# Optimization experiments

Measured on AMD Instinct MI355X. Metric: run time of the kernel, lower is better.

Reference implementation:

```python
import jax, jax.numpy as jnp
import numpy as np

B, LI, LT, DM, H = 1, 2048, 384, 2560, 20
DH = DM // H  # 128
EPS = 1e-05


def _rms(x, w):
    # torch.nn.RMSNorm over last dim (inner_dim), elementwise affine w
    return x * jax.lax.rsqrt(jnp.mean(x * x, axis=-1, keepdims=True) + EPS) * w


def _apply_rope(x, rope):
    # x: [B, L, H, D]; rope: [1, L, 1, D/2, 2, 2] (flux-style freqs_cis)
    xr = x.reshape(x.shape[0], x.shape[1], x.shape[2], -1, 1, 2)  # [B,L,H,D/2,1,2]
    out = rope[..., 0] * xr[..., 0] + rope[..., 1] * xr[..., 1]   # [B,L,H,D/2,2]
    return out.reshape(x.shape)


def _sdpa(q, k, v):
    # q,k,v: [B, L, H, D] -> out [B, L, H*D]; scale 1/sqrt(D)
    scale = 1.0 / np.sqrt(q.shape[-1]).astype(np.float32)
    scores = jnp.einsum('bqhd,bkhd->bhqk', q, k) * scale
    p = jax.nn.softmax(scores, axis=-1)
    o = jnp.einsum('bhqk,bkhd->bqhd', p, v)
    return o.reshape(o.shape[0], o.shape[1], -1)


def _lin(x, W, b):
    return x @ W.T + b


def _forward(img, txt, rope, img_masks,
             Wq, bq, Wk, bk, Wv, bv, Wo, bo, qn, kn,
             Wq_t, bq_t, Wk_t, bk_t, Wv_t, bv_t, Wo_t, bo_t, qn_t, kn_t):
    bsz = img.shape[0]
    # img stream: proj -> RMSNorm -> head split
    iq = _rms(_lin(img, Wq, bq), qn).reshape(bsz, -1, H, DH)
    ik = _rms(_lin(img, Wk, bk), kn).reshape(bsz, -1, H, DH)
    iv = _lin(img, Wv, bv).reshape(bsz, -1, H, DH)
    ik = ik * img_masks[:, :, None, None]
    # txt stream
    tq = _rms(_lin(txt, Wq_t, bq_t), qn_t).reshape(bsz, -1, H, DH)
    tk = _rms(_lin(txt, Wk_t, bk_t), kn_t).reshape(bsz, -1, H, DH)
    tv = _lin(txt, Wv_t, bv_t).reshape(bsz, -1, H, DH)
    # concat streams, apply rope, attention
    q = jnp.concatenate([iq, tq], axis=1)
    k = jnp.concatenate([ik, tk], axis=1)
    v = jnp.concatenate([iv, tv], axis=1)
    q = _apply_rope(q, rope)
    k = _apply_rope(k, rope)
    attn = _sdpa(q, k, v)  # [B, LI+LT, DM]
    img_attn, txt_attn = attn[:, :LI], attn[:, LI:]
    return _lin(img_attn, Wo, bo), _lin(txt_attn, Wo_t, bo_t)


def setup_inputs() -> dict:
    key = jax.random.key(0)
    ks = jax.random.split(key, 16)
    s = 0.02
    inp = {
        'img': jax.random.normal(ks[0], (B, LI, DM), jnp.float32),
        'txt': jax.random.normal(ks[1], (B, LT, DM), jnp.float32),
        'rope': jax.random.normal(ks[2], (1, LI + LT, 1, DH // 2, 2, 2), jnp.float32),
        'img_masks': jnp.ones((B, LI), jnp.float32),
    }
    wnames = ['Wq', 'Wk', 'Wv', 'Wo', 'Wq_t', 'Wk_t', 'Wv_t', 'Wo_t']
    for i, n in enumerate(wnames):
        inp[n] = jax.random.normal(ks[3 + i], (DM, DM), jnp.float32) * s
        inp['b' + n[1:]] = jnp.zeros((DM,), jnp.float32)
    for i, n in enumerate(['qn', 'kn', 'qn_t', 'kn_t']):
        inp[n] = jax.random.uniform(ks[11 + i], (DM,), jnp.float32, 0.5, 1.5)
    return inp


def reference(img, txt, rope, img_masks,
              Wq, bq, Wk, bk, Wv, bv, Wo, bo, qn, kn,
              Wq_t, bq_t, Wk_t, bk_t, Wv_t, bv_t, Wo_t, bo_t, qn_t, kn_t):
    return _forward(img, txt, rope, img_masks,
                    Wq, bq, Wk, bk, Wv, bv, Wo, bo, qn, kn,
                    Wq_t, bq_t, Wk_t, bk_t, Wv_t, bv_t, Wo_t, bo_t, qn_t, kn_t)
```

## Files before the change

### kernel.cpp

```cpp
#include <hip/hip_runtime.h>
#include <math.h>

#define LI 2048
#define LT 384
#define LSEQ 2432
#define DM 2560
#define NH 20
#define DH 128
#define SCALE 0.08838834764831845f
#define NKV 38

typedef __bf16 bf16x8 __attribute__((ext_vector_type(8)));
typedef __bf16 bf16x4 __attribute__((ext_vector_type(4)));
typedef __bf16 bf16x2 __attribute__((ext_vector_type(2)));
typedef float f32x4 __attribute__((ext_vector_type(4)));
typedef float f32x16 __attribute__((ext_vector_type(16)));

__device__ __forceinline__ void async_copy16(const void* gsrc, void* lds_uniform) {
    __builtin_amdgcn_global_load_lds(
        (const __attribute__((address_space(1))) unsigned int*)gsrc,
        (__attribute__((address_space(3))) unsigned int*)lds_uniform,
        16, 0, 0);
}


__global__ __launch_bounds__(256) void cvt8_kernel(
    const float* __restrict__ s0, const float* __restrict__ s1,
    const float* __restrict__ s2, const float* __restrict__ s3,
    const float* __restrict__ s4, const float* __restrict__ s5,
    const float* __restrict__ s6, const float* __restrict__ s7,
    __bf16* __restrict__ dst)
{
    const float* srcs[8] = {s0, s1, s2, s3, s4, s5, s6, s7};
    const float* s = srcs[blockIdx.y];
    __bf16* d = dst + (size_t)blockIdx.y * (size_t)DM * DM;
    int i = blockIdx.x * 256 + threadIdx.x;
    const float4* sp = (const float4*)s + (size_t)i * 2;
    float4 a = sp[0], b = sp[1];
    bf16x8 o = {(__bf16)a.x, (__bf16)a.y, (__bf16)a.z, (__bf16)a.w,
                (__bf16)b.x, (__bf16)b.y, (__bf16)b.z, (__bf16)b.w};
    *((bf16x8*)d + i) = o;
}

__global__ __launch_bounds__(256) void cvt_kernel(
    const float* __restrict__ s, __bf16* __restrict__ d, int n8)
{
    int i = blockIdx.x * 256 + threadIdx.x;
    if (i >= n8) return;
    const float4* sp = (const float4*)s + (size_t)i * 2;
    float4 a = sp[0], b = sp[1];
    bf16x8 o = {(__bf16)a.x, (__bf16)a.y, (__bf16)a.z, (__bf16)a.w,
                (__bf16)b.x, (__bf16)b.y, (__bf16)b.z, (__bf16)b.w};
    *((bf16x8*)d + i) = o;
}


__device__ __forceinline__ void gemm_core(
    const __bf16* __restrict__ Ab,
    const __bf16* __restrict__ Bb,
    const float* __restrict__ bias,
    float* __restrict__ Cb,
    __bf16* sA, __bf16* sB)
{
    const int t = threadIdx.x, wave = t >> 6, lane = t & 63;
    const int l15 = lane & 15, quad = lane >> 4;
    const int wm = wave >> 1, wn = wave & 1;

    f32x4 acc[4][4];
#pragma unroll
    for (int i = 0; i < 4; i++)
#pragma unroll
        for (int j = 0; j < 4; j++) acc[i][j] = f32x4{0.f, 0.f, 0.f, 0.f};

    size_t soff[4];
#pragma unroll
    for (int j = 0; j < 4; j++) {
        int c = j * 256 + t;
        int row = c >> 3, u = c & 7;
        soff[j] = (size_t)row * DM + ((u ^ (row & 7)) * 8);
    }

    for (int k0 = 0; k0 < DM; k0 += 64) {
        __syncthreads();
#pragma unroll
        for (int j = 0; j < 4; j++)
            async_copy16(Ab + soff[j] + k0, (char*)sA + (j * 256 + wave * 64) * 16);
#pragma unroll
        for (int j = 0; j < 4; j++)
            async_copy16(Bb + soff[j] + k0, (char*)sB + (j * 256 + wave * 64) * 16);
        __syncthreads();

#pragma unroll
        for (int ks = 0; ks < 2; ks++) {
            bf16x8 af[4], bg[4];
#pragma unroll
            for (int mt = 0; mt < 4; mt++) {
                int r = wm * 64 + mt * 16 + l15;
                af[mt] = *(const bf16x8*)(sA + r * 64 + (((quad + ks * 4) ^ (r & 7)) * 8));
            }
#pragma unroll
            for (int nt = 0; nt < 4; nt++) {
                int r = wn * 64 + nt * 16 + l15;
                bg[nt] = *(const bf16x8*)(sB + r * 64 + (((quad + ks * 4) ^ (r & 7)) * 8));
            }
#pragma unroll
            for (int mt = 0; mt < 4; mt++)
#pragma unroll
                for (int nt = 0; nt < 4; nt++)
                    acc[mt][nt] = __builtin_amdgcn_mfma_f32_16x16x32_bf16(af[mt], bg[nt], acc[mt][nt], 0, 0, 0);
        }
    }

#pragma unroll
    for (int mt = 0; mt < 4; mt++) {
        const int row = wm * 64 + mt * 16 + quad * 4;
#pragma unroll
        for (int nt = 0; nt < 4; nt++) {
            const int col = wn * 64 + nt * 16 + l15;
            const float bv = bias[col];
            float* cp = Cb + (size_t)row * DM + col;
            cp[0]        = acc[mt][nt][0] + bv;
            cp[DM]       = acc[mt][nt][1] + bv;
            cp[2 * DM]   = acc[mt][nt][2] + bv;
            cp[3 * DM]   = acc[mt][nt][3] + bv;
        }
    }
}

__device__ __forceinline__ void qkv_body(
    int nblk, int mblk,
    const __bf16* __restrict__ xbf, const __bf16* __restrict__ wbf,
    const float* __restrict__ bq, const float* __restrict__ bk, const float* __restrict__ bv,
    const float* __restrict__ bq_t, const float* __restrict__ bk_t, const float* __restrict__ bv_t,
    float* __restrict__ qraw, float* __restrict__ kraw, float* __restrict__ vraw,
    __bf16* sA, __bf16* sB)
{
    const int which = nblk / 20;
    const int nloc = (nblk % 20) * 128;
    const bool is_txt = (mblk >= 16);
    const size_t WELEM = (size_t)DM * DM;
    const int widx = which + (is_txt ? 4 : 0);
    const __bf16* W = wbf + (size_t)widx * WELEM;
    const float* bias = (which == 0) ? (is_txt ? bq_t : bq)
                      : (which == 1) ? (is_txt ? bk_t : bk)
                                     : (is_txt ? bv_t : bv);
    float* C = (which == 0) ? qraw : (which == 1) ? kraw : vraw;
    gemm_core(xbf + (size_t)mblk * 128 * DM, W + (size_t)nloc * DM, bias + nloc,
              C + (size_t)mblk * 128 * DM + nloc, sA, sB);
}

__global__ __launch_bounds__(256, 4) void gemm_qkv_a_kernel(
    const __bf16* __restrict__ xbf, const __bf16* __restrict__ wbf,
    const float* __restrict__ bq, const float* __restrict__ bk, const float* __restrict__ bv,
    const float* __restrict__ bq_t, const float* __restrict__ bk_t, const float* __restrict__ bv_t,
    float* __restrict__ qraw, float* __restrict__ kraw, float* __restrict__ vraw)
{
    __shared__ alignas(16) __bf16 sA[128 * 64];
    __shared__ alignas(16) __bf16 sB[128 * 64];
    qkv_body(blockIdx.x, blockIdx.y, xbf, wbf, bq, bk, bv, bq_t, bk_t, bv_t,
             qraw, kraw, vraw, sA, sB);
}

__global__ __launch_bounds__(256, 4) void gemm_qkv_b_kernel(
    const __bf16* __restrict__ xbf, const __bf16* __restrict__ wbf,
    const float* __restrict__ bq, const float* __restrict__ bk, const float* __restrict__ bv,
    const float* __restrict__ bq_t, const float* __restrict__ bk_t, const float* __restrict__ bv_t,
    float* __restrict__ qraw, float* __restrict__ kraw, float* __restrict__ vraw)
{
    __shared__ alignas(16) __bf16 sA[128 * 64];
    __shared__ alignas(16) __bf16 sB[128 * 64];
    qkv_body(blockIdx.x, blockIdx.y + 10, xbf, wbf, bq, bk, bv, bq_t, bk_t, bv_t,
             qraw, kraw, vraw, sA, sB);
}

__global__ __launch_bounds__(256, 4) void gemm_out_kernel(
    const __bf16* __restrict__ attnbf, const __bf16* __restrict__ wbf,
    const float* __restrict__ bo, const float* __restrict__ bo_t,
    float* __restrict__ out)
{
    __shared__ alignas(16) __bf16 sA[128 * 64];
    __shared__ alignas(16) __bf16 sB[128 * 64];
    const int nblk = blockIdx.x, mblk = blockIdx.y;
    const bool is_txt = (mblk >= 16);
    const size_t WELEM = (size_t)DM * DM;
    const __bf16* W = wbf + (size_t)(is_txt ? 7 : 3) * WELEM;
    const float* bias = (is_txt ? bo_t : bo) + nblk * 128;
    gemm_core(attnbf + (size_t)mblk * 128 * DM, W + (size_t)nblk * 128 * DM, bias,
              out + (size_t)mblk * 128 * DM + nblk * 128, sA, sB);
}


__global__ __launch_bounds__(256) void rmsrope_kernel(
    const float* __restrict__ qraw, const float* __restrict__ kraw,
    const float* __restrict__ rope, const float* __restrict__ img_masks,
    const float* __restrict__ qn, const float* __restrict__ kn,
    const float* __restrict__ qn_t, const float* __restrict__ kn_t,
    __bf16* __restrict__ qbf, __bf16* __restrict__ kbf)
{
    const int l = blockIdx.x, t = threadIdx.x;
    const int wave = t >> 6, lane = t & 63;
    const bool is_img = (l < LI);
    const float* qw = is_img ? qn : qn_t;
    const float* kw = is_img ? kn : kn_t;
    const float kmask = is_img ? img_masks[l] : 1.0f;
    const float* qr = qraw + (size_t)l * DM;
    const float* kr = kraw + (size_t)l * DM;

    float2 qv[5], kv[5];
    float sq = 0.f, sk = 0.f;
#pragma unroll
    for (int j = 0; j < 5; j++) {
        int c2 = j * 256 + t;
        qv[j] = *(const float2*)(qr + 2 * c2);
        kv[j] = *(const float2*)(kr + 2 * c2);
        sq += qv[j].x * qv[j].x + qv[j].y * qv[j].y;
        sk += kv[j].x * kv[j].x + kv[j].y * kv[j].y;
    }
#pragma unroll
    for (int m = 32; m; m >>= 1) { sq += __shfl_xor(sq, m); sk += __shfl_xor(sk, m); }
    __shared__ float redq[4], redk[4];
    if (lane == 0) { redq[wave] = sq; redk[wave] = sk; }
    __syncthreads();
    sq = redq[0] + redq[1] + redq[2] + redq[3];
    sk = redk[0] + redk[1] + redk[2] + redk[3];
    const float rq = rsqrtf(sq * (1.0f / DM) + 1e-5f);
    const float rk = rsqrtf(sk * (1.0f / DM) + 1e-5f) * kmask;

#pragma unroll
    for (int j = 0; j < 5; j++) {
        int c2 = j * 256 + t;
        int c = 2 * c2;
        float4 rp = *(const float4*)(rope + ((size_t)l * 64 + (c2 & 63)) * 4);
        float2 w2q = *(const float2*)(qw + c);
        float2 w2k = *(const float2*)(kw + c);
        float x0 = qv[j].x * rq * w2q.x, x1 = qv[j].y * rq * w2q.y;
        bf16x2 oq = {(__bf16)(rp.x * x0 + rp.y * x1), (__bf16)(rp.z * x0 + rp.w * x1)};
        *(bf16x2*)(qbf + (size_t)l * DM + c) = oq;
        float y0 = kv[j].x * rk * w2k.x, y1 = kv[j].y * rk * w2k.y;
        bf16x2 ok = {(__bf16)(rp.x * y0 + rp.y * y1), (__bf16)(rp.z * y0 + rp.w * y1)};
        *(bf16x2*)(kbf + (size_t)l * DM + c) = ok;
    }
}


__global__ __launch_bounds__(256) void transpose_cvt_kernel(
    const float* __restrict__ src, __bf16* __restrict__ dst)
{
    __shared__ float tile[32][33];
    const int c0 = blockIdx.x * 32;
    const int r0 = blockIdx.y * 32;
    const int tc = threadIdx.x & 31, tr = threadIdx.x >> 5;
#pragma unroll
    for (int j = 0; j < 4; j++)
        tile[tr + j * 8][tc] = src[(size_t)(r0 + tr + j * 8) * DM + c0 + tc];
    __syncthreads();
#pragma unroll
    for (int j = 0; j < 4; j++)
        dst[(size_t)(c0 + tr + j * 8) * LSEQ + r0 + tc] = (__bf16)tile[tc][tr + j * 8];
}


__global__ __launch_bounds__(256, 3) void flash_kernel(
    const __bf16* __restrict__ qb, const __bf16* __restrict__ kb,
    const __bf16* __restrict__ vt, __bf16* __restrict__ ob)
{
    __shared__ alignas(16) char smem[34816];
    const int head = blockIdx.x;
    const int q0 = blockIdx.y * 64;
    const int t = threadIdx.x, wave = t >> 6, lane = t & 63;
    const int s = wave >> 1, h = wave & 1;
    const int l31 = lane & 31, h5 = lane >> 5;

    bf16x8 bq8[8];
    {
        const __bf16* qp = qb + (size_t)(q0 + s * 32 + l31) * DM + head * DH;
#pragma unroll
        for (int t8 = 0; t8 < 8; t8++)
            bq8[t8] = *(const bf16x8*)(qp + t8 * 16 + h5 * 8);
    }

    int koff[4], voff[4];
#pragma unroll
    for (int j = 0; j < 4; j++) {
        int c = j * 256 + t;
        int krow = c >> 4, ku = (c & 15) ^ (krow & 7);
        koff[j] = krow * DM + head * DH + ku * 8;
        int vrow = c >> 3, vu = (c & 7) ^ (vrow & 7);
        voff[j] = (head * DH + vrow) * LSEQ + vu * 8;
    }
    const int dunit = wave * 1024;

    const __bf16* sK = (const __bf16*)smem;
    const __bf16* sV = (const __bf16*)(smem + 16384);
    const int kbase = 32 * h;

    f32x16 o[4];
#pragma unroll
    for (int dt = 0; dt < 4; dt++)
#pragma unroll
        for (int e = 0; e < 16; e++) o[dt][e] = 0.f;
    float m_i = -INFINITY, l_i = 0.f;

    for (int it = 0; it < NKV; ++it) {
        __syncthreads();
#pragma unroll
        for (int j = 0; j < 4; j++) {
            async_copy16(kb + koff[j] + (size_t)(it * 64) * DM, smem + j * 4096 + dunit);
            async_copy16(vt + voff[j] + it * 64, smem + 16384 + j * 4096 + dunit);
        }
        __syncthreads();

        f32x16 st;
#pragma unroll
        for (int e = 0; e < 16; e++) st[e] = 0.f;
        __builtin_amdgcn_s_setprio(1);
#pragma unroll
        for (int t8 = 0; t8 < 8; t8++) {
            int row = kbase + l31;
            int unit = (2 * t8 + h5) ^ (row & 7);
            bf16x8 ak = *(const bf16x8*)(sK + row * 128 + unit * 8);
            st = __builtin_amdgcn_mfma_f32_32x32x16_bf16(ak, bq8[t8], st, 0, 0, 0);
        }
        __builtin_amdgcn_s_setprio(0);

        float mx = m_i;
#pragma unroll
        for (int e = 0; e < 16; e++) { st[e] *= SCALE; mx = fmaxf(mx, st[e]); }
        mx = fmaxf(mx, __shfl_xor(mx, 32));
        const float al = __expf(m_i - mx);
        m_i = mx;
        float sum = 0.f;
#pragma unroll
        for (int e = 0; e < 16; e++) { float p = __expf(st[e] - mx); st[e] = p; sum += p; }
        sum += __shfl_xor(sum, 32);
        l_i = l_i * al + sum;
#pragma unroll
        for (int dt = 0; dt < 4; dt++)
#pragma unroll
            for (int e = 0; e < 16; e++) o[dt][e] *= al;

        bf16x8 pfrag[2];
#pragma unroll
        for (int c = 0; c < 2; c++) {
            union { bf16x2 v; unsigned u; } A, B, C, D;
            A.v = bf16x2{(__bf16)st[8 * c + 0], (__bf16)st[8 * c + 1]};
            B.v = bf16x2{(__bf16)st[8 * c + 2], (__bf16)st[8 * c + 3]};
            C.v = bf16x2{(__bf16)st[8 * c + 4], (__bf16)st[8 * c + 5]};
            D.v = bf16x2{(__bf16)st[8 * c + 6], (__bf16)st[8 * c + 7]};
            unsigned xA = __shfl_xor(A.u, 32), xB = __shfl_xor(B.u, 32);
            unsigned xC = __shfl_xor(C.u, 32), xD = __shfl_xor(D.u, 32);
            union { unsigned w[4]; bf16x8 v; } pf;
            pf.w[0] = h5 ? xC : A.u;
            pf.w[1] = h5 ? xD : B.u;
            pf.w[2] = h5 ? C.u : xA;
            pf.w[3] = h5 ? D.u : xB;
            pfrag[c] = pf.v;
        }

        __builtin_amdgcn_s_setprio(1);
#pragma unroll
        for (int dt = 0; dt < 4; dt++) {
            int row = dt * 32 + l31;
#pragma unroll
            for (int c = 0; c < 2; c++) {
                int unit = (4 * h + 2 * c + h5) ^ (row & 7);
                bf16x8 av = *(const bf16x8*)(sV + row * 64 + unit * 8);
                o[dt] = __builtin_amdgcn_mfma_f32_32x32x16_bf16(av, pfrag[c], o[dt], 0, 0, 0);
            }
        }
        __builtin_amdgcn_s_setprio(0);
    }

    __syncthreads();
    float* mlbuf = (float*)(smem + 33792);
    if (lane < 32) {
        mlbuf[((s * 2 + h) * 2 + 0) * 32 + lane] = m_i;
        mlbuf[((s * 2 + h) * 2 + 1) * 32 + lane] = l_i;
    }
    __syncthreads();
    const float pm = mlbuf[((s * 2 + (h ^ 1)) * 2 + 0) * 32 + l31];
    const float pl = mlbuf[((s * 2 + (h ^ 1)) * 2 + 1) * 32 + l31];
    const float M = fmaxf(m_i, pm);
    const float sc = __expf(m_i - M), psc = __expf(pm - M);
    const float L = l_i * sc + pl * psc;
    const float fac = sc / L;
    float* obuf = (float*)smem + s * 4224;
    if (h == 1) {
#pragma unroll
        for (int dt = 0; dt < 4; dt++)
#pragma unroll
            for (int e = 0; e < 16; e++) {
                int dout = dt * 32 + (e & 3) + 8 * (e >> 2) + 4 * h5;
                obuf[l31 * 132 + dout] = o[dt][e] * fac;
            }
    }
    __syncthreads();
    if (h == 0) {
#pragma unroll
        for (int dt = 0; dt < 4; dt++)
#pragma unroll
            for (int e = 0; e < 16; e++) {
                int dout = dt * 32 + (e & 3) + 8 * (e >> 2) + 4 * h5;
                int idx = l31 * 132 + dout;
                obuf[idx] = o[dt][e] * fac + obuf[idx];
            }
    }
    __syncthreads();
#pragma unroll
    for (int rr = 0; rr < 8; rr++) {
        int qblk = wave * 16 + h5 * 8 + rr;
        int ss = qblk >> 5, qq = qblk & 31;
        const float* src = (const float*)smem + ss * 4224 + qq * 132 + l31 * 4;
        float4 v4 = *(const float4*)src;
        bf16x4 ov = {(__bf16)v4.x, (__bf16)v4.y, (__bf16)v4.z, (__bf16)v4.w};
        *(bf16x4*)(ob + (size_t)(q0 + qblk) * DM + head * DH + l31 * 4) = ov;
    }
}


extern "C" void kernel_launch(void* const* d_in, const int* in_sizes, int n_in,
                              void* d_out, int out_size, void* d_ws, size_t ws_size,
                              hipStream_t stream) {
    const float* img       = (const float*)d_in[0];
    const float* txt       = (const float*)d_in[1];
    const float* rope      = (const float*)d_in[2];
    const float* img_masks = (const float*)d_in[3];
    const float* Wq   = (const float*)d_in[4];  const float* bq   = (const float*)d_in[5];
    const float* Wk   = (const float*)d_in[6];  const float* bk   = (const float*)d_in[7];
    const float* Wv   = (const float*)d_in[8];  const float* bv   = (const float*)d_in[9];
    const float* Wo   = (const float*)d_in[10]; const float* bo   = (const float*)d_in[11];
    const float* Wq_t = (const float*)d_in[12]; const float* bq_t = (const float*)d_in[13];
    const float* Wk_t = (const float*)d_in[14]; const float* bk_t = (const float*)d_in[15];
    const float* Wv_t = (const float*)d_in[16]; const float* bv_t = (const float*)d_in[17];
    const float* Wo_t = (const float*)d_in[18]; const float* bo_t = (const float*)d_in[19];
    const float* qn   = (const float*)d_in[20]; const float* kn   = (const float*)d_in[21];
    const float* qn_t = (const float*)d_in[22]; const float* kn_t = (const float*)d_in[23];
    float* out = (float*)d_out;

    const size_t WELEM = (size_t)DM * DM;
    const size_t XELEM = (size_t)LSEQ * DM;

    __bf16* wbf  = (__bf16*)d_ws;
    __bf16* xbf  = wbf + 8 * WELEM;
    float*  qraw = (float*)(xbf + XELEM);
    float*  kraw = qraw + XELEM;
    float*  vraw = kraw + XELEM;
    __bf16* qbf  = (__bf16*)(vraw + XELEM);
    __bf16* kbf  = qbf + XELEM;
    __bf16* vt   = kbf + XELEM;
    __bf16* attnbf = (__bf16*)qraw;

    cvt8_kernel<<<dim3((int)(WELEM / 8 / 256), 8), 256, 0, stream>>>(
        Wq, Wk, Wv, Wo, Wq_t, Wk_t, Wv_t, Wo_t, wbf);
    cvt_kernel<<<dim3((LI * DM / 8 + 255) / 256), 256, 0, stream>>>(img, xbf, LI * DM / 8);
    cvt_kernel<<<dim3((LT * DM / 8 + 255) / 256), 256, 0, stream>>>(
        txt, xbf + (size_t)LI * DM, LT * DM / 8);

    gemm_qkv_a_kernel<<<dim3(60, 10), 256, 0, stream>>>(
        xbf, wbf, bq, bk, bv, bq_t, bk_t, bv_t, qraw, kraw, vraw);
    gemm_qkv_b_kernel<<<dim3(60, 9), 256, 0, stream>>>(
        xbf, wbf, bq, bk, bv, bq_t, bk_t, bv_t, qraw, kraw, vraw);

    rmsrope_kernel<<<dim3(LSEQ), 256, 0, stream>>>(
        qraw, kraw, rope, img_masks, qn, kn, qn_t, kn_t, qbf, kbf);

    transpose_cvt_kernel<<<dim3(DM / 32, LSEQ / 32), 256, 0, stream>>>(vraw, vt);

    flash_kernel<<<dim3(NH, LSEQ / 64), 256, 0, stream>>>(qbf, kbf, vt, attnbf);

    gemm_out_kernel<<<dim3(20, 19), 256, 0, stream>>>(attnbf, wbf, bo, bo_t, out);
}
```

Baseline: 583.7 us.

## Double-buffer K tiles in flash attention, lazy rescale with exp2, merge QKV GEMM launches

```diff
diff --git a/kernel.cpp b/kernel.cpp
--- a/kernel.cpp
+++ b/kernel.cpp
@@ -8,6 +8,7 @@
 #define NH 20
 #define DH 128
 #define SCALE 0.08838834764831845f
+#define CEXP (SCALE * 1.4426950408889634f)
 #define NKV 38
 
 typedef __bf16 bf16x8 __attribute__((ext_vector_type(8)));
@@ -127,14 +128,15 @@
     }
 }
 
-__device__ __forceinline__ void qkv_body(
-    int nblk, int mblk,
+__global__ __launch_bounds__(256, 4) void gemm_qkv_kernel(
     const __bf16* __restrict__ xbf, const __bf16* __restrict__ wbf,
     const float* __restrict__ bq, const float* __restrict__ bk, const float* __restrict__ bv,
     const float* __restrict__ bq_t, const float* __restrict__ bk_t, const float* __restrict__ bv_t,
-    float* __restrict__ qraw, float* __restrict__ kraw, float* __restrict__ vraw,
-    __bf16* sA, __bf16* sB)
-{
+    float* __restrict__ qraw, float* __restrict__ kraw, float* __restrict__ vraw)
+{
+    __shared__ alignas(16) __bf16 sA[128 * 64];
+    __shared__ alignas(16) __bf16 sB[128 * 64];
+    const int nblk = blockIdx.x, mblk = blockIdx.y;
     const int which = nblk / 20;
     const int nloc = (nblk % 20) * 128;
     const bool is_txt = (mblk >= 16);
@@ -149,30 +151,6 @@
               C + (size_t)mblk * 128 * DM + nloc, sA, sB);
 }
 
-__global__ __launch_bounds__(256, 4) void gemm_qkv_a_kernel(
-    const __bf16* __restrict__ xbf, const __bf16* __restrict__ wbf,
-    const float* __restrict__ bq, const float* __restrict__ bk, const float* __restrict__ bv,
-    const float* __restrict__ bq_t, const float* __restrict__ bk_t, const float* __restrict__ bv_t,
-    float* __restrict__ qraw, float* __restrict__ kraw, float* __restrict__ vraw)
-{
-    __shared__ alignas(16) __bf16 sA[128 * 64];
-    __shared__ alignas(16) __bf16 sB[128 * 64];
-    qkv_body(blockIdx.x, blockIdx.y, xbf, wbf, bq, bk, bv, bq_t, bk_t, bv_t,
-             qraw, kraw, vraw, sA, sB);
-}
-
-__global__ __launch_bounds__(256, 4) void gemm_qkv_b_kernel(
-    const __bf16* __restrict__ xbf, const __bf16* __restrict__ wbf,
-    const float* __restrict__ bq, const float* __restrict__ bk, const float* __restrict__ bv,
-    const float* __restrict__ bq_t, const float* __restrict__ bk_t, const float* __restrict__ bv_t,
-    float* __restrict__ qraw, float* __restrict__ kraw, float* __restrict__ vraw)
-{
-    __shared__ alignas(16) __bf16 sA[128 * 64];
-    __shared__ alignas(16) __bf16 sB[128 * 64];
-    qkv_body(blockIdx.x, blockIdx.y + 10, xbf, wbf, bq, bk, bv, bq_t, bk_t, bv_t,
-             qraw, kraw, vraw, sA, sB);
-}
-
 __global__ __launch_bounds__(256, 4) void gemm_out_kernel(
     const __bf16* __restrict__ attnbf, const __bf16* __restrict__ wbf,
     const float* __restrict__ bo, const float* __restrict__ bo_t,
@@ -264,7 +242,7 @@
     const __bf16* __restrict__ qb, const __bf16* __restrict__ kb,
     const __bf16* __restrict__ vt, __bf16* __restrict__ ob)
 {
-    __shared__ alignas(16) char smem[34816];
+    __shared__ alignas(16) char smem[49152];
     const int head = blockIdx.x;
     const int q0 = blockIdx.y * 64;
     const int t = threadIdx.x, wave = t >> 6, lane = t & 63;
@@ -289,9 +267,6 @@
         voff[j] = (head * DH + vrow) * LSEQ + vu * 8;
     }
     const int dunit = wave * 1024;
-
-    const __bf16* sK = (const __bf16*)smem;
-    const __bf16* sV = (const __bf16*)(smem + 16384);
     const int kbase = 32 * h;
 
     f32x16 o[4];
@@ -299,16 +274,21 @@
     for (int dt = 0; dt < 4; dt++)
 #pragma unroll
         for (int e = 0; e < 16; e++) o[dt][e] = 0.f;
-    float m_i = -INFINITY, l_i = 0.f;
+    float m_i = -INFINITY, l_i = 0.f, mc = 0.f;
+
+#pragma unroll
+    for (int j = 0; j < 4; j++)
+        async_copy16(kb + koff[j], smem + j * 4096 + dunit);
 
     for (int it = 0; it < NKV; ++it) {
-        __syncthreads();
-#pragma unroll
-        for (int j = 0; j < 4; j++) {
-            async_copy16(kb + koff[j] + (size_t)(it * 64) * DM, smem + j * 4096 + dunit);
-            async_copy16(vt + voff[j] + it * 64, smem + 16384 + j * 4096 + dunit);
-        }
-        __syncthreads();
+        const __bf16* sK = (const __bf16*)(smem + (it & 1) * 16384);
+        const __bf16* sV = (const __bf16*)(smem + 32768);
+
+        asm volatile("s_waitcnt vmcnt(0)\n\ts_barrier" ::: "memory");
+
+#pragma unroll
+        for (int j = 0; j < 4; j++)
+            async_copy16(vt + voff[j] + it * 64, smem + 32768 + j * 4096 + dunit);
 
         f32x16 st;
 #pragma unroll
@@ -323,21 +303,37 @@
         }
         __builtin_amdgcn_s_setprio(0);
 
-        float mx = m_i;
-#pragma unroll
-        for (int e = 0; e < 16; e++) { st[e] *= SCALE; mx = fmaxf(mx, st[e]); }
-        mx = fmaxf(mx, __shfl_xor(mx, 32));
-        const float al = __expf(m_i - mx);
-        m_i = mx;
+        float pmax = st[0];
+#pragma unroll
+        for (int e = 1; e < 16; e++) pmax = fmaxf(pmax, st[e]);
+        pmax = fmaxf(pmax, __shfl_xor(pmax, 32));
+        if (!__all(pmax <= m_i + 90.0f)) {
+            const float mnew = fmaxf(m_i, pmax);
+            const float al = exp2f((m_i - mnew) * CEXP);
+            m_i = mnew; mc = mnew * CEXP;
+#pragma unroll
+            for (int dt = 0; dt < 4; dt++)
+#pragma unroll
+                for (int e = 0; e < 16; e++) o[dt][e] *= al;
+            l_i *= al;
+        }
         float sum = 0.f;
 #pragma unroll
-        for (int e = 0; e < 16; e++) { float p = __expf(st[e] - mx); st[e] = p; sum += p; }
+        for (int e = 0; e < 16; e++) {
+            float p = exp2f(st[e] * CEXP - mc);
+            st[e] = p; sum += p;
+        }
         sum += __shfl_xor(sum, 32);
-        l_i = l_i * al + sum;
-#pragma unroll
-        for (int dt = 0; dt < 4; dt++)
-#pragma unroll
-            for (int e = 0; e < 16; e++) o[dt][e] *= al;
+        l_i += sum;
+
+        asm volatile("s_waitcnt vmcnt(0)\n\ts_barrier" ::: "memory");
+
+        if (it + 1 < NKV) {
+#pragma unroll
+            for (int j = 0; j < 4; j++)
+                async_copy16(kb + koff[j] + (size_t)((it + 1) * 64) * DM,
+                             smem + ((it + 1) & 1) * 16384 + j * 4096 + dunit);
+        }
 
         bf16x8 pfrag[2];
 #pragma unroll
@@ -381,7 +377,7 @@
     const float pm = mlbuf[((s * 2 + (h ^ 1)) * 2 + 0) * 32 + l31];
     const float pl = mlbuf[((s * 2 + (h ^ 1)) * 2 + 1) * 32 + l31];
     const float M = fmaxf(m_i, pm);
-    const float sc = __expf(m_i - M), psc = __expf(pm - M);
+    const float sc = exp2f((m_i - M) * CEXP), psc = exp2f((pm - M) * CEXP);
     const float L = l_i * sc + pl * psc;
     const float fac = sc / L;
     float* obuf = (float*)smem + s * 4224;
@@ -456,9 +452,7 @@
     cvt_kernel<<<dim3((LT * DM / 8 + 255) / 256), 256, 0, stream>>>(
         txt, xbf + (size_t)LI * DM, LT * DM / 8);
 
-    gemm_qkv_a_kernel<<<dim3(60, 10), 256, 0, stream>>>(
-        xbf, wbf, bq, bk, bv, bq_t, bk_t, bv_t, qraw, kraw, vraw);
-    gemm_qkv_b_kernel<<<dim3(60, 9), 256, 0, stream>>>(
+    gemm_qkv_kernel<<<dim3(60, 19), 256, 0, stream>>>(
         xbf, wbf, bq, bk, bv, bq_t, bk_t, bv_t, qraw, kraw, vraw);
 
     rmsrope_kernel<<<dim3(LSEQ), 256, 0, stream>>>(
```

Result: no change. 579.4 us (-0.7%).
